# Kernel tuning notes

Hardware: AMD Instinct MI355X
Metric: run time of the kernel (lower is better)

The kernel has to match this reference:

```python
import jax, jax.numpy as jnp
import numpy as np

N_NODES = 50000
N_EDGES = 640000
D = 128
N_RELS = 16
N_NTYPES = 8


def setup_inputs() -> dict:
    key = jax.random.key(0)
    ks = jax.random.split(key, 9)
    return {
        "feats": jax.random.normal(ks[0], (N_NODES, D), dtype=jnp.float32),
        "W_edge": jax.random.normal(ks[1], (N_RELS, D, D), dtype=jnp.float32) / np.sqrt(D),
        "b_edge": jax.random.normal(ks[2], (N_RELS, D), dtype=jnp.float32) * 0.02,
        "W_node": jax.random.normal(ks[3], (N_NTYPES, D, D), dtype=jnp.float32) / np.sqrt(D),
        "b_node": jax.random.normal(ks[4], (N_NTYPES, D), dtype=jnp.float32) * 0.02,
        "src": jax.random.randint(ks[5], (N_EDGES,), 0, N_NODES, dtype=jnp.int32),
        "dst": jax.random.randint(ks[6], (N_EDGES,), 0, N_NODES, dtype=jnp.int32),
        "ntypes": jax.random.randint(ks[7], (N_NODES,), 0, N_NTYPES, dtype=jnp.int32),
        "etypes": jax.random.randint(ks[8], (N_EDGES,), 0, N_RELS, dtype=jnp.int32),
    }


def reference(feats, W_edge, b_edge, W_node, b_node, src, dst, ntypes, etypes):
    N, d = feats.shape
    T = W_edge.shape[0]
    # Per-relation linear applied to all nodes once: [T, N, out]; then gather per edge.
    hW = jnp.einsum('nd,tdf->tnf', feats, W_edge) + b_edge[:, None, :]
    msg = hW[etypes, src]  # [E, out]
    # Per-(dst-node, edge-type) in-degree counts (one_hot count normalization).
    seg = dst * T + etypes  # [E]
    counts = jax.ops.segment_sum(jnp.ones(msg.shape[0], dtype=msg.dtype), seg,
                                 num_segments=N * T)  # [N*T]
    msg = msg / counts[seg][:, None]
    # Scatter-sum messages into destination nodes (zero for isolated nodes).
    agg = jax.ops.segment_sum(msg, dst, num_segments=N)  # [N, out]
    # Type-conditional node transform + residual message + activation.
    hN = jnp.einsum('nd,tdf->tnf', feats, W_node) + b_node[:, None, :]  # [Tn, N, out]
    out = hN[ntypes, jnp.arange(N)] + agg
    return jax.nn.relu(out)
```

## Files before the change

kernel.cpp:

```cpp
#include <hip/hip_runtime.h>
#include <hip/hip_bf16.h>
#include <stdint.h>


#define D 128
#define TRELS 16
#define NTYPES 8

typedef __bf16 bf16x8 __attribute__((ext_vector_type(8)));
typedef float f32x4 __attribute__((ext_vector_type(4)));

__device__ __forceinline__ unsigned short f2bf(float f) {
  union { float f; unsigned u; } v; v.f = f;
  unsigned u = v.u;
  return (unsigned short)((u + 0x7FFFu + ((u >> 16) & 1u)) >> 16);
}
__device__ __forceinline__ float bf2f(unsigned short h) {
  union { unsigned u; float f; } v; v.u = ((unsigned)h) << 16;
  return v.f;
}

__global__ void prep_k(const float* __restrict__ feats,
                       const float* __restrict__ We,
                       const float* __restrict__ Wn,
                       unsigned short* __restrict__ featsbf,
                       unsigned short* __restrict__ WeT,
                       unsigned short* __restrict__ WnT,
                       int nfeat) {
  int idx = blockIdx.x * 256 + threadIdx.x;
  if (idx < nfeat) { featsbf[idx] = f2bf(feats[idx]); return; }
  idx -= nfeat;
  if (idx < TRELS * D * D) {
    int t = idx >> 14, rem = idx & 16383;
    int n = rem >> 7, k = rem & 127;
    WeT[idx] = f2bf(We[t * 16384 + k * 128 + n]);
    return;
  }
  idx -= TRELS * D * D;
  if (idx < NTYPES * D * D) {
    int t = idx >> 14, rem = idx & 16383;
    int n = rem >> 7, k = rem & 127;
    WnT[idx] = f2bf(Wn[t * 16384 + k * 128 + n]);
  }
}

__global__ void hist_k(const int* __restrict__ dst, const int* __restrict__ etypes,
                       const int* __restrict__ ntypes, int E, int N,
                       int* __restrict__ cnt, int* __restrict__ nhist) {
  __shared__ int sh_n[NTYPES];
  int tid = threadIdx.x;
  if (tid < NTYPES) sh_n[tid] = 0;
  __syncthreads();
  int g = blockIdx.x * 256 + tid;
  if (g < E) atomicAdd(&cnt[dst[g] * TRELS + etypes[g]], 1);
  if (g < N) atomicAdd(&sh_n[ntypes[g]], 1);
  __syncthreads();
  if (tid < NTYPES && sh_n[tid]) atomicAdd(&nhist[tid], sh_n[tid]);
}

__global__ void scan1_k(const int* __restrict__ cnt, int* __restrict__ doff,
                        int* __restrict__ bsum, int N) {
  __shared__ int sd[256];
  int b = blockIdx.x, tid = threadIdx.x;
  int base = b * 1024 + tid * 4;
  int v[4]; int tot = 0;
  for (int j = 0; j < 4; ++j) {
    int i = base + j;
    int dg = 0;
    if (i < N) {
      const int* row = cnt + i * TRELS;
#pragma unroll
      for (int et = 0; et < TRELS; ++et) dg += row[et];
    }
    v[j] = tot; tot += dg;
  }
  sd[tid] = tot;
  __syncthreads();
  for (int off = 1; off < 256; off <<= 1) {
    int t = (tid >= off) ? sd[tid - off] : 0;
    __syncthreads();
    sd[tid] += t;
    __syncthreads();
  }
  int excl = sd[tid] - tot;
  for (int j = 0; j < 4; ++j) {
    int i = base + j;
    if (i < N) doff[i] = excl + v[j];
  }
  if (tid == 255) bsum[b] = sd[255];
}

__global__ void scan2_k(int* __restrict__ misc, int* __restrict__ bsum, int nb) {
  if (threadIdx.x != 0) return;
  int run = 0;
  for (int b = 0; b < nb; ++b) { int t = bsum[b]; bsum[b] = run; run += t; }
  int* noff = misc; int* ntb = misc + 9; int* ncur = misc + 18; int* nhist = misc + 26;
  int s = 0, ts = 0;
  for (int t = 0; t < NTYPES; ++t) {
    noff[t] = s; ncur[t] = s; ntb[t] = ts;
    s += nhist[t]; ts += (nhist[t] + 127) >> 7;
  }
  noff[NTYPES] = s; ntb[NTYPES] = ts;
}

__global__ void scan3_k(int* __restrict__ doff, int* __restrict__ dcur,
                        const int* __restrict__ bsum, int N, int E) {
  int b = blockIdx.x, tid = threadIdx.x;
  int add = bsum[b];
  int base = b * 1024 + tid * 4;
  for (int j = 0; j < 4; ++j) {
    int i = base + j;
    if (i < N) { int o = doff[i] + add; doff[i] = o; dcur[i] = o; }
  }
  if (b == 0 && tid == 0) doff[N] = E;
}

__global__ void scatter_k(const int* __restrict__ src, const int* __restrict__ dst,
                          const int* __restrict__ etypes, const int* __restrict__ ntypes,
                          int E, int N, int* __restrict__ misc,
                          int* __restrict__ dcur,
                          int* __restrict__ edst, int* __restrict__ nsorted) {
  __shared__ int lc_n[NTYPES], lb_n[NTYPES];
  int tid = threadIdx.x;
  if (tid < NTYPES) lc_n[tid] = 0;
  __syncthreads();
  int g = blockIdx.x * 256 + tid;
  if (g < E) {
    int d = dst[g];
    int pos = atomicAdd(&dcur[d], 1);
    edst[pos] = src[g] * TRELS + etypes[g];
  }
  int tn = -1, idn = 0;
  if (g < N) { tn = ntypes[g]; idn = atomicAdd(&lc_n[tn], 1); }
  __syncthreads();
  if (tid < NTYPES && lc_n[tid]) lb_n[tid] = atomicAdd(&misc[18 + tid], lc_n[tid]);
  __syncthreads();
  if (g < N) nsorted[lb_n[tn] + idn] = g;
}

__global__ __launch_bounds__(256) void hw_gemm_k(
    const unsigned short* __restrict__ featsbf,
    const unsigned short* __restrict__ WeT,
    unsigned short* __restrict__ hW, int N) {
  __shared__ unsigned char Asm[128 * 264];
  int tid = threadIdx.x;
  int et = blockIdx.y;
  int tile = blockIdx.x;

  int lane = tid & 63, w = tid >> 6;
  int m = lane & 15, q = lane >> 4;
  int rw = (w & 1) * 64, cw = (w >> 1) * 64;

  const unsigned short* WB = WeT + et * (D * D);
  bf16x8 bfr[4][4];
#pragma unroll
  for (int ks = 0; ks < 4; ++ks)
#pragma unroll
    for (int j = 0; j < 4; ++j)
      bfr[ks][j] = *reinterpret_cast<const bf16x8*>(WB + (cw + j * 16 + m) * D + ks * 32 + q * 8);

  int r = tid >> 1, h = tid & 1;
  int row = tile * 128 + r;
  if (row < N) {
    const uint4* gp = reinterpret_cast<const uint4*>(featsbf + (size_t)row * D);
#pragma unroll
    for (int cc = 0; cc < 8; ++cc) {
      int c = h * 8 + cc;
      *reinterpret_cast<uint4*>(&Asm[r * 256 + ((c ^ (r & 7)) << 4)]) = gp[c];
    }
  }
  __syncthreads();

  f32x4 acc[4][4];
#pragma unroll
  for (int i = 0; i < 4; ++i)
#pragma unroll
    for (int j = 0; j < 4; ++j) acc[i][j] = (f32x4){0.f, 0.f, 0.f, 0.f};

#pragma unroll
  for (int ks = 0; ks < 4; ++ks) {
    bf16x8 a[4];
#pragma unroll
    for (int i = 0; i < 4; ++i) {
      int rr = rw + i * 16 + m;
      int c = ks * 4 + q;
      a[i] = *reinterpret_cast<const bf16x8*>(&Asm[rr * 256 + ((c ^ (rr & 7)) << 4)]);
    }
#pragma unroll
    for (int i = 0; i < 4; ++i)
#pragma unroll
      for (int j = 0; j < 4; ++j)
        acc[i][j] = __builtin_amdgcn_mfma_f32_16x16x32_bf16(a[i], bfr[ks][j], acc[i][j], 0, 0, 0);
  }

  __syncthreads();
  unsigned short* Cs = reinterpret_cast<unsigned short*>(Asm);
#pragma unroll
  for (int i = 0; i < 4; ++i)
#pragma unroll
    for (int j = 0; j < 4; ++j)
#pragma unroll
      for (int reg = 0; reg < 4; ++reg) {
        int rr = rw + i * 16 + q * 4 + reg;
        Cs[rr * 132 + cw + j * 16 + m] = f2bf(acc[i][j][reg]);
      }
  __syncthreads();
  char* gout = (char*)(hW + ((size_t)et * N + (size_t)tile * 128) * D);
#pragma unroll
  for (int cp = 0; cp < 8; ++cp) {
    int o = cp * 4096 + tid * 16;
    int rloc = o >> 8;
    if (tile * 128 + rloc < N) {
      uint4 v = *reinterpret_cast<const uint4*>(&Asm[rloc * 264 + (o & 255)]);
      *reinterpret_cast<uint4*>(gout + o) = v;
    }
  }
}

__global__ __launch_bounds__(256) void agg_k(
    const unsigned short* __restrict__ hW,
    const float* __restrict__ b_edge,
    const int* __restrict__ cnt,
    const int* __restrict__ doff, const int* __restrict__ edst,
    float* __restrict__ agg, int N) {
  int tid = threadIdx.x;
  int lane = tid & 63, w = tid >> 6;
  int d = blockIdx.x * 4 + w;
  if (d >= N) return;

  int cv = 0;
  if (lane < TRELS) cv = cnt[d * TRELS + lane];
  float invl = (cv > 0) ? 1.0f / (float)cv : 0.0f;

  int start = doff[d], end = doff[d + 1];
  float ax = 0.f, ay = 0.f;
  for (int base = start; base < end; base += 64) {
    int key = 0;
    if (base + lane < end) key = edst[base + lane];
    int nchunk = end - base; if (nchunk > 64) nchunk = 64;
    int j = 0;
    for (; j + 4 <= nchunk; j += 4) {
      int k0 = __shfl(key, j, 64), k1 = __shfl(key, j + 1, 64);
      int k2 = __shfl(key, j + 2, 64), k3 = __shfl(key, j + 3, 64);
      float i0 = __shfl(invl, k0 & 15, 64), i1 = __shfl(invl, k1 & 15, 64);
      float i2 = __shfl(invl, k2 & 15, 64), i3 = __shfl(invl, k3 & 15, 64);
      ushort2 h0 = *reinterpret_cast<const ushort2*>(hW + ((size_t)(k0 & 15) * N + (k0 >> 4)) * D + lane * 2);
      ushort2 h1 = *reinterpret_cast<const ushort2*>(hW + ((size_t)(k1 & 15) * N + (k1 >> 4)) * D + lane * 2);
      ushort2 h2 = *reinterpret_cast<const ushort2*>(hW + ((size_t)(k2 & 15) * N + (k2 >> 4)) * D + lane * 2);
      ushort2 h3 = *reinterpret_cast<const ushort2*>(hW + ((size_t)(k3 & 15) * N + (k3 >> 4)) * D + lane * 2);
      ax += i0 * bf2f(h0.x); ay += i0 * bf2f(h0.y);
      ax += i1 * bf2f(h1.x); ay += i1 * bf2f(h1.y);
      ax += i2 * bf2f(h2.x); ay += i2 * bf2f(h2.y);
      ax += i3 * bf2f(h3.x); ay += i3 * bf2f(h3.y);
    }
    for (; j < nchunk; ++j) {
      int k = __shfl(key, j, 64);
      float inv = __shfl(invl, k & 15, 64);
      ushort2 hv = *reinterpret_cast<const ushort2*>(hW + ((size_t)(k & 15) * N + (k >> 4)) * D + lane * 2);
      ax += inv * bf2f(hv.x); ay += inv * bf2f(hv.y);
    }
  }
#pragma unroll
  for (int et = 0; et < TRELS; ++et) {
    int c = __shfl(cv, et, 64);
    if (c > 0) {
      const float* bp = b_edge + et * D + lane * 2;
      ax += bp[0]; ay += bp[1];
    }
  }
  float2* op = reinterpret_cast<float2*>(agg + (size_t)d * D + lane * 2);
  *op = make_float2(ax, ay);
}

__global__ __launch_bounds__(256) void node_gemm_k(
    const unsigned short* __restrict__ featsbf,
    const unsigned short* __restrict__ WnT,
    const float* __restrict__ b_node,
    const int* __restrict__ nsorted, const int* __restrict__ misc,
    const float* __restrict__ agg,
    float* __restrict__ out) {
  __shared__ unsigned char Asm[128 * 264];
  __shared__ int sm_node[128];
  __shared__ int s_ntb[9];
  int tid = threadIdx.x;
  if (tid < 9) s_ntb[tid] = misc[9 + tid];
  __syncthreads();
  int bid = blockIdx.x;
  if (bid >= s_ntb[8]) return;
  int t = 0;
  while (bid >= s_ntb[t + 1]) ++t;
  int tile = bid - s_ntb[t];
  int noff_t = misc[t];
  int cntT = misc[t + 1] - noff_t;

  int lane = tid & 63, w = tid >> 6;
  int m = lane & 15, q = lane >> 4;
  int rw = (w & 1) * 64, cw = (w >> 1) * 64;

  const unsigned short* WB = WnT + t * (D * D);
  bf16x8 bfr[4][4];
#pragma unroll
  for (int ks = 0; ks < 4; ++ks)
#pragma unroll
    for (int j = 0; j < 4; ++j)
      bfr[ks][j] = *reinterpret_cast<const bf16x8*>(WB + (cw + j * 16 + m) * D + ks * 32 + q * 8);

  int r = tid >> 1, h = tid & 1;
  int gidx = tile * 128 + r;
  bool rv = gidx < cntT;
  int node = 0;
  if (rv) node = nsorted[noff_t + gidx];
  if (h == 0) sm_node[r] = rv ? node : -1;
  if (rv) {
    const uint4* gp = reinterpret_cast<const uint4*>(featsbf + (size_t)node * D);
#pragma unroll
    for (int cc = 0; cc < 8; ++cc) {
      int c = h * 8 + cc;
      *reinterpret_cast<uint4*>(&Asm[r * 256 + ((c ^ (r & 7)) << 4)]) = gp[c];
    }
  }
  __syncthreads();

  f32x4 acc[4][4];
#pragma unroll
  for (int i = 0; i < 4; ++i)
#pragma unroll
    for (int j = 0; j < 4; ++j) acc[i][j] = (f32x4){0.f, 0.f, 0.f, 0.f};

#pragma unroll
  for (int ks = 0; ks < 4; ++ks) {
    bf16x8 a[4];
#pragma unroll
    for (int i = 0; i < 4; ++i) {
      int rr = rw + i * 16 + m;
      int c = ks * 4 + q;
      a[i] = *reinterpret_cast<const bf16x8*>(&Asm[rr * 256 + ((c ^ (rr & 7)) << 4)]);
    }
#pragma unroll
    for (int i = 0; i < 4; ++i)
#pragma unroll
      for (int j = 0; j < 4; ++j)
        acc[i][j] = __builtin_amdgcn_mfma_f32_16x16x32_bf16(a[i], bfr[ks][j], acc[i][j], 0, 0, 0);
  }

  const float* bnp = b_node + t * D;
  float* Cf = reinterpret_cast<float*>(Asm);
  __syncthreads();
#pragma unroll
  for (int half = 0; half < 2; ++half) {
    if ((w & 1) == half) {
#pragma unroll
      for (int i = 0; i < 4; ++i)
#pragma unroll
        for (int j = 0; j < 4; ++j)
#pragma unroll
          for (int reg = 0; reg < 4; ++reg) {
            int rl = i * 16 + q * 4 + reg;
            Cf[rl * 132 + cw + j * 16 + m] = acc[i][j][reg];
          }
    }
    __syncthreads();
#pragma unroll
    for (int cp = 0; cp < 8; ++cp) {
      int o = cp * 4096 + tid * 16;
      int rl = o >> 9;
      int nd = sm_node[half * 64 + rl];
      if (nd >= 0) {
        int col = (o & 511) >> 2;
        f32x4 c = *reinterpret_cast<const f32x4*>((char*)Cf + rl * 528 + (o & 511));
        f32x4 a = *reinterpret_cast<const f32x4*>(agg + (size_t)nd * D + col);
        f32x4 b4 = *reinterpret_cast<const f32x4*>(bnp + col);
        f32x4 res;
#pragma unroll
        for (int z = 0; z < 4; ++z) res[z] = fmaxf(c[z] + a[z] + b4[z], 0.f);
        *reinterpret_cast<f32x4*>(out + (size_t)nd * D + col) = res;
      }
    }
    __syncthreads();
  }
}

static inline size_t align256(size_t x) { return (x + 255) & ~(size_t)255; }

extern "C" void kernel_launch(void* const* d_in, const int* in_sizes, int n_in,
                              void* d_out, int out_size, void* d_ws, size_t ws_size,
                              hipStream_t stream) {
  const float* feats  = (const float*)d_in[0];
  const float* W_edge = (const float*)d_in[1];
  const float* b_edge = (const float*)d_in[2];
  const float* W_node = (const float*)d_in[3];
  const float* b_node = (const float*)d_in[4];
  const int* src    = (const int*)d_in[5];
  const int* dst    = (const int*)d_in[6];
  const int* ntypes = (const int*)d_in[7];
  const int* etypes = (const int*)d_in[8];
  int N = in_sizes[0] / D;
  int E = in_sizes[5];

  char* ws = (char*)d_ws;
  size_t o_cnt  = 0;
  size_t o_misc = align256(o_cnt + (size_t)N * TRELS * 4);
  size_t zend   = align256(o_misc + 512);
  size_t o_doff = zend;
  size_t o_dcur = align256(o_doff + (size_t)(N + 1) * 4);
  size_t o_edst = align256(o_dcur + (size_t)N * 4);
  size_t o_ns   = align256(o_edst + (size_t)E * 4);
  size_t o_fb   = align256(o_ns + (size_t)N * 4);
  size_t o_we   = align256(o_fb + (size_t)N * D * 2);
  size_t o_wn   = align256(o_we + (size_t)TRELS * D * D * 2);
  size_t o_agg  = align256(o_wn + (size_t)NTYPES * D * D * 2);
  size_t o_hw   = align256(o_agg + (size_t)N * D * 4);

  int* cnt = (int*)(ws + o_cnt);
  int* misc = (int*)(ws + o_misc);
  int* doff = (int*)(ws + o_doff);
  int* dcur = (int*)(ws + o_dcur);
  int* edst = (int*)(ws + o_edst);
  int* nsorted = (int*)(ws + o_ns);
  unsigned short* featsbf = (unsigned short*)(ws + o_fb);
  unsigned short* WeT = (unsigned short*)(ws + o_we);
  unsigned short* WnT = (unsigned short*)(ws + o_wn);
  float* agg = (float*)(ws + o_agg);
  unsigned short* hW = (unsigned short*)(ws + o_hw);
  int* bsum = misc + 64;

  hipMemsetAsync(ws, 0, zend, stream);

  int nfeat = N * D;
  int ptot = nfeat + TRELS * D * D + NTYPES * D * D;
  prep_k<<<(ptot + 255) / 256, 256, 0, stream>>>(feats, W_edge, W_node, featsbf, WeT, WnT, nfeat);

  int hgrid = ((E > N ? E : N) + 255) / 256;
  hist_k<<<hgrid, 256, 0, stream>>>(dst, etypes, ntypes, E, N, cnt, misc + 26);

  int nb = (N + 1023) / 1024;
  scan1_k<<<nb, 256, 0, stream>>>(cnt, doff, bsum, N);
  scan2_k<<<1, 64, 0, stream>>>(misc, bsum, nb);
  scan3_k<<<nb, 256, 0, stream>>>(doff, dcur, bsum, N, E);

  scatter_k<<<hgrid, 256, 0, stream>>>(src, dst, etypes, ntypes, E, N, misc, dcur, edst, nsorted);

  int mtiles = (N + 127) / 128;
  dim3 ggrid(mtiles, TRELS);
  hw_gemm_k<<<ggrid, 256, 0, stream>>>(featsbf, WeT, hW, N);

  agg_k<<<(N + 3) / 4, 256, 0, stream>>>(hW, b_edge, cnt, doff, edst, agg, N);

  int ngrid = mtiles + NTYPES;
  node_gemm_k<<<ngrid, 256, 0, stream>>>(featsbf, WnT, b_node, nsorted, misc, agg, (float*)d_out);
}
```

Baseline: 344.5 us.

## Remap hw_gemm blocks per XCD, use nontemporal stores, widen agg gathers

Measured after the change: 347.4 us. Within noise of the previous version (+0.8%).

```diff
diff --git a/kernel.cpp b/kernel.cpp
--- a/kernel.cpp
+++ b/kernel.cpp
@@ -9,6 +9,7 @@
 
 typedef __bf16 bf16x8 __attribute__((ext_vector_type(8)));
 typedef float f32x4 __attribute__((ext_vector_type(4)));
+typedef unsigned int u32x4 __attribute__((ext_vector_type(4)));
 
 __device__ __forceinline__ unsigned short f2bf(float f) {
   union { float f; unsigned u; } v; v.f = f;
@@ -18,6 +19,11 @@
 __device__ __forceinline__ float bf2f(unsigned short h) {
   union { unsigned u; float f; } v; v.u = ((unsigned)h) << 16;
   return v.f;
+}
+__device__ __forceinline__ void bfpair(unsigned u, float& lo, float& hi) {
+  union { unsigned u; float f; } a, b;
+  a.u = u << 16; b.u = u & 0xffff0000u;
+  lo = a.f; hi = b.f;
 }
 
 __global__ void prep_k(const float* __restrict__ feats,
@@ -141,14 +147,20 @@
 __global__ __launch_bounds__(256) void hw_gemm_k(
     const unsigned short* __restrict__ featsbf,
     const unsigned short* __restrict__ WeT,
-    unsigned short* __restrict__ hW, int N) {
+    unsigned short* __restrict__ hW, int N, int mtiles) {
   __shared__ unsigned char Asm[128 * 264];
   int tid = threadIdx.x;
-  int et = blockIdx.y;
-  int tile = blockIdx.x;
+
+  int G = mtiles * 16;
+  int q = G >> 3, rmod = G & 7;
+  int xcd = blockIdx.x & 7, bidx = blockIdx.x >> 3;
+  int wrk = (xcd < rmod) ? (xcd * (q + 1) + bidx)
+                         : (rmod * (q + 1) + (xcd - rmod) * q + bidx);
+  int tile = wrk >> 4;
+  int et = wrk & 15;
 
   int lane = tid & 63, w = tid >> 6;
-  int m = lane & 15, q = lane >> 4;
+  int m = lane & 15, qd = lane >> 4;
   int rw = (w & 1) * 64, cw = (w >> 1) * 64;
 
   const unsigned short* WB = WeT + et * (D * D);
@@ -157,16 +169,16 @@
   for (int ks = 0; ks < 4; ++ks)
 #pragma unroll
     for (int j = 0; j < 4; ++j)
-      bfr[ks][j] = *reinterpret_cast<const bf16x8*>(WB + (cw + j * 16 + m) * D + ks * 32 + q * 8);
+      bfr[ks][j] = *reinterpret_cast<const bf16x8*>(WB + (cw + j * 16 + m) * D + ks * 32 + qd * 8);
 
   int r = tid >> 1, h = tid & 1;
   int row = tile * 128 + r;
   if (row < N) {
-    const uint4* gp = reinterpret_cast<const uint4*>(featsbf + (size_t)row * D);
+    const u32x4* gp = reinterpret_cast<const u32x4*>(featsbf + (size_t)row * D);
 #pragma unroll
     for (int cc = 0; cc < 8; ++cc) {
       int c = h * 8 + cc;
-      *reinterpret_cast<uint4*>(&Asm[r * 256 + ((c ^ (r & 7)) << 4)]) = gp[c];
+      *reinterpret_cast<u32x4*>(&Asm[r * 256 + ((c ^ (r & 7)) << 4)]) = gp[c];
     }
   }
   __syncthreads();
@@ -183,7 +195,7 @@
 #pragma unroll
     for (int i = 0; i < 4; ++i) {
       int rr = rw + i * 16 + m;
-      int c = ks * 4 + q;
+      int c = ks * 4 + qd;
       a[i] = *reinterpret_cast<const bf16x8*>(&Asm[rr * 256 + ((c ^ (rr & 7)) << 4)]);
     }
 #pragma unroll
@@ -201,7 +213,7 @@
     for (int j = 0; j < 4; ++j)
 #pragma unroll
       for (int reg = 0; reg < 4; ++reg) {
-        int rr = rw + i * 16 + q * 4 + reg;
+        int rr = rw + i * 16 + qd * 4 + reg;
         Cs[rr * 132 + cw + j * 16 + m] = f2bf(acc[i][j][reg]);
       }
   __syncthreads();
@@ -211,8 +223,8 @@
     int o = cp * 4096 + tid * 16;
     int rloc = o >> 8;
     if (tile * 128 + rloc < N) {
-      uint4 v = *reinterpret_cast<const uint4*>(&Asm[rloc * 264 + (o & 255)]);
-      *reinterpret_cast<uint4*>(gout + o) = v;
+      u32x4 v = *reinterpret_cast<const u32x4*>(&Asm[rloc * 264 + (o & 255)]);
+      __builtin_nontemporal_store(v, reinterpret_cast<u32x4*>(gout + o));
     }
   }
 }
@@ -232,44 +244,56 @@
   if (lane < TRELS) cv = cnt[d * TRELS + lane];
   float invl = (cv > 0) ? 1.0f / (float)cv : 0.0f;
 
+  int g = lane >> 4;
+  int sub = lane & 15;
+
   int start = doff[d], end = doff[d + 1];
-  float ax = 0.f, ay = 0.f;
+  float acc[8];
+#pragma unroll
+  for (int z = 0; z < 8; ++z) acc[z] = 0.f;
+
   for (int base = start; base < end; base += 64) {
     int key = 0;
     if (base + lane < end) key = edst[base + lane];
     int nchunk = end - base; if (nchunk > 64) nchunk = 64;
-    int j = 0;
-    for (; j + 4 <= nchunk; j += 4) {
-      int k0 = __shfl(key, j, 64), k1 = __shfl(key, j + 1, 64);
-      int k2 = __shfl(key, j + 2, 64), k3 = __shfl(key, j + 3, 64);
-      float i0 = __shfl(invl, k0 & 15, 64), i1 = __shfl(invl, k1 & 15, 64);
-      float i2 = __shfl(invl, k2 & 15, 64), i3 = __shfl(invl, k3 & 15, 64);
-      ushort2 h0 = *reinterpret_cast<const ushort2*>(hW + ((size_t)(k0 & 15) * N + (k0 >> 4)) * D + lane * 2);
-      ushort2 h1 = *reinterpret_cast<const ushort2*>(hW + ((size_t)(k1 & 15) * N + (k1 >> 4)) * D + lane * 2);
-      ushort2 h2 = *reinterpret_cast<const ushort2*>(hW + ((size_t)(k2 & 15) * N + (k2 >> 4)) * D + lane * 2);
-      ushort2 h3 = *reinterpret_cast<const ushort2*>(hW + ((size_t)(k3 & 15) * N + (k3 >> 4)) * D + lane * 2);
-      ax += i0 * bf2f(h0.x); ay += i0 * bf2f(h0.y);
-      ax += i1 * bf2f(h1.x); ay += i1 * bf2f(h1.y);
-      ax += i2 * bf2f(h2.x); ay += i2 * bf2f(h2.y);
-      ax += i3 * bf2f(h3.x); ay += i3 * bf2f(h3.y);
-    }
-    for (; j < nchunk; ++j) {
-      int k = __shfl(key, j, 64);
+#pragma unroll 2
+    for (int j = 0; j < nchunk; j += 4) {
+      int rr = j + g;
+      int k = __shfl(key, rr, 64);
       float inv = __shfl(invl, k & 15, 64);
-      ushort2 hv = *reinterpret_cast<const ushort2*>(hW + ((size_t)(k & 15) * N + (k >> 4)) * D + lane * 2);
-      ax += inv * bf2f(hv.x); ay += inv * bf2f(hv.y);
-    }
-  }
+      if (rr < nchunk) {
+        const unsigned short* hp =
+            hW + ((size_t)(k & 15) * N + (size_t)(k >> 4)) * D + sub * 8;
+        u32x4 hv = *reinterpret_cast<const u32x4*>(hp);
+        float lo, hi;
+        bfpair(hv.x, lo, hi); acc[0] += inv * lo; acc[1] += inv * hi;
+        bfpair(hv.y, lo, hi); acc[2] += inv * lo; acc[3] += inv * hi;
+        bfpair(hv.z, lo, hi); acc[4] += inv * lo; acc[5] += inv * hi;
+        bfpair(hv.w, lo, hi); acc[6] += inv * lo; acc[7] += inv * hi;
+      }
+    }
+  }
+
+#pragma unroll
+  for (int z = 0; z < 8; ++z) {
+    acc[z] += __shfl_xor(acc[z], 16, 64);
+    acc[z] += __shfl_xor(acc[z], 32, 64);
+  }
+
+  int cb = sub * 8 + (g & 1) * 4;
+  f32x4 res = { acc[(g & 1) * 4 + 0], acc[(g & 1) * 4 + 1],
+                acc[(g & 1) * 4 + 2], acc[(g & 1) * 4 + 3] };
 #pragma unroll
   for (int et = 0; et < TRELS; ++et) {
     int c = __shfl(cv, et, 64);
     if (c > 0) {
-      const float* bp = b_edge + et * D + lane * 2;
-      ax += bp[0]; ay += bp[1];
-    }
-  }
-  float2* op = reinterpret_cast<float2*>(agg + (size_t)d * D + lane * 2);
-  *op = make_float2(ax, ay);
+      f32x4 b4 = *reinterpret_cast<const f32x4*>(b_edge + et * D + cb);
+#pragma unroll
+      for (int z = 0; z < 4; ++z) res[z] += b4[z];
+    }
+  }
+  if (g < 2)
+    *reinterpret_cast<f32x4*>(agg + (size_t)d * D + cb) = res;
 }
 
 __global__ __launch_bounds__(256) void node_gemm_k(
@@ -312,11 +336,11 @@
   if (rv) node = nsorted[noff_t + gidx];
   if (h == 0) sm_node[r] = rv ? node : -1;
   if (rv) {
-    const uint4* gp = reinterpret_cast<const uint4*>(featsbf + (size_t)node * D);
+    const u32x4* gp = reinterpret_cast<const u32x4*>(featsbf + (size_t)node * D);
 #pragma unroll
     for (int cc = 0; cc < 8; ++cc) {
       int c = h * 8 + cc;
-      *reinterpret_cast<uint4*>(&Asm[r * 256 + ((c ^ (r & 7)) << 4)]) = gp[c];
+      *reinterpret_cast<u32x4*>(&Asm[r * 256 + ((c ^ (r & 7)) << 4)]) = gp[c];
     }
   }
   __syncthreads();
@@ -424,7 +448,7 @@
   unsigned short* hW = (unsigned short*)(ws + o_hw);
   int* bsum = misc + 64;
 
-  hipMemsetAsync(ws, 0, zend, stream);
+  (void)hipMemsetAsync(ws, 0, zend, stream);
 
   int nfeat = N * D;
   int ptot = nfeat + TRELS * D * D + NTYPES * D * D;
@@ -441,8 +465,7 @@
   scatter_k<<<hgrid, 256, 0, stream>>>(src, dst, etypes, ntypes, E, N, misc, dcur, edst, nsorted);
 
   int mtiles = (N + 127) / 128;
-  dim3 ggrid(mtiles, TRELS);
-  hw_gemm_k<<<ggrid, 256, 0, stream>>>(featsbf, WeT, hW, N);
+  hw_gemm_k<<<mtiles * 16, 256, 0, stream>>>(featsbf, WeT, hW, N, mtiles);
 
   agg_k<<<(N + 3) / 4, 256, 0, stream>>>(hW, b_edge, cnt, doff, edst, agg, N);
 
```

## Skip storing unused per-relation hW rows and remap GEMM blocks per XCD

Applied to the files above, without the earlier changes.

Result: no change. 349.5 us (+1.4%).

```diff
diff --git a/kernel.cpp b/kernel.cpp
--- a/kernel.cpp
+++ b/kernel.cpp
@@ -9,6 +9,7 @@
 
 typedef __bf16 bf16x8 __attribute__((ext_vector_type(8)));
 typedef float f32x4 __attribute__((ext_vector_type(4)));
+typedef unsigned int u32x4 __attribute__((ext_vector_type(4)));
 
 __device__ __forceinline__ unsigned short f2bf(float f) {
   union { float f; unsigned u; } v; v.f = f;
@@ -44,15 +45,21 @@
   }
 }
 
-__global__ void hist_k(const int* __restrict__ dst, const int* __restrict__ etypes,
+__global__ void hist_k(const int* __restrict__ src, const int* __restrict__ dst,
+                       const int* __restrict__ etypes,
                        const int* __restrict__ ntypes, int E, int N,
-                       int* __restrict__ cnt, int* __restrict__ nhist) {
+                       int* __restrict__ cnt, int* __restrict__ nhist,
+                       int* __restrict__ srcuse) {
   __shared__ int sh_n[NTYPES];
   int tid = threadIdx.x;
   if (tid < NTYPES) sh_n[tid] = 0;
   __syncthreads();
   int g = blockIdx.x * 256 + tid;
-  if (g < E) atomicAdd(&cnt[dst[g] * TRELS + etypes[g]], 1);
+  if (g < E) {
+    int et = etypes[g];
+    atomicAdd(&cnt[dst[g] * TRELS + et], 1);
+    atomicOr(&srcuse[src[g]], 1 << et);
+  }
   if (g < N) atomicAdd(&sh_n[ntypes[g]], 1);
   __syncthreads();
   if (tid < NTYPES && sh_n[tid]) atomicAdd(&nhist[tid], sh_n[tid]);
@@ -141,32 +148,45 @@
 __global__ __launch_bounds__(256) void hw_gemm_k(
     const unsigned short* __restrict__ featsbf,
     const unsigned short* __restrict__ WeT,
-    unsigned short* __restrict__ hW, int N) {
+    const int* __restrict__ srcuse,
+    unsigned short* __restrict__ hW, int N, int mtiles) {
   __shared__ unsigned char Asm[128 * 264];
+  __shared__ unsigned char sm_use[128];
   int tid = threadIdx.x;
-  int et = blockIdx.y;
-  int tile = blockIdx.x;
+
+  int G = mtiles * 16;
+  int q = G >> 3, rmod = G & 7;
+  int xcd = blockIdx.x & 7, bidx = blockIdx.x >> 3;
+  int wrk = (xcd < rmod) ? (xcd * (q + 1) + bidx)
+                         : (rmod * (q + 1) + (xcd - rmod) * q + bidx);
+  int tile = wrk >> 4;
+  int et = wrk & 15;
 
   int lane = tid & 63, w = tid >> 6;
-  int m = lane & 15, q = lane >> 4;
+  int m = lane & 15, qd = lane >> 4;
   int rw = (w & 1) * 64, cw = (w >> 1) * 64;
 
-  const unsigned short* WB = WeT + et * (D * D);
+  const unsigned short* WB = WeT + (size_t)et * (D * D);
   bf16x8 bfr[4][4];
 #pragma unroll
   for (int ks = 0; ks < 4; ++ks)
 #pragma unroll
     for (int j = 0; j < 4; ++j)
-      bfr[ks][j] = *reinterpret_cast<const bf16x8*>(WB + (cw + j * 16 + m) * D + ks * 32 + q * 8);
+      bfr[ks][j] = *reinterpret_cast<const bf16x8*>(WB + (cw + j * 16 + m) * D + ks * 32 + qd * 8);
+
+  if (tid < 128) {
+    int rowu = tile * 128 + tid;
+    sm_use[tid] = (rowu < N) ? (unsigned char)((srcuse[rowu] >> et) & 1) : 0;
+  }
 
   int r = tid >> 1, h = tid & 1;
   int row = tile * 128 + r;
   if (row < N) {
-    const uint4* gp = reinterpret_cast<const uint4*>(featsbf + (size_t)row * D);
+    const u32x4* gp = reinterpret_cast<const u32x4*>(featsbf + (size_t)row * D);
 #pragma unroll
     for (int cc = 0; cc < 8; ++cc) {
       int c = h * 8 + cc;
-      *reinterpret_cast<uint4*>(&Asm[r * 256 + ((c ^ (r & 7)) << 4)]) = gp[c];
+      *reinterpret_cast<u32x4*>(&Asm[r * 256 + ((c ^ (r & 7)) << 4)]) = gp[c];
     }
   }
   __syncthreads();
@@ -183,7 +203,7 @@
 #pragma unroll
     for (int i = 0; i < 4; ++i) {
       int rr = rw + i * 16 + m;
-      int c = ks * 4 + q;
+      int c = ks * 4 + qd;
       a[i] = *reinterpret_cast<const bf16x8*>(&Asm[rr * 256 + ((c ^ (rr & 7)) << 4)]);
     }
 #pragma unroll
@@ -201,7 +221,7 @@
     for (int j = 0; j < 4; ++j)
 #pragma unroll
       for (int reg = 0; reg < 4; ++reg) {
-        int rr = rw + i * 16 + q * 4 + reg;
+        int rr = rw + i * 16 + qd * 4 + reg;
         Cs[rr * 132 + cw + j * 16 + m] = f2bf(acc[i][j][reg]);
       }
   __syncthreads();
@@ -210,9 +230,9 @@
   for (int cp = 0; cp < 8; ++cp) {
     int o = cp * 4096 + tid * 16;
     int rloc = o >> 8;
-    if (tile * 128 + rloc < N) {
-      uint4 v = *reinterpret_cast<const uint4*>(&Asm[rloc * 264 + (o & 255)]);
-      *reinterpret_cast<uint4*>(gout + o) = v;
+    if (tile * 128 + rloc < N && sm_use[rloc]) {
+      u32x4 v = *reinterpret_cast<const u32x4*>(&Asm[rloc * 264 + (o & 255)]);
+      *reinterpret_cast<u32x4*>(gout + o) = v;
     }
   }
 }
@@ -312,11 +332,11 @@
   if (rv) node = nsorted[noff_t + gidx];
   if (h == 0) sm_node[r] = rv ? node : -1;
   if (rv) {
-    const uint4* gp = reinterpret_cast<const uint4*>(featsbf + (size_t)node * D);
+    const u32x4* gp = reinterpret_cast<const u32x4*>(featsbf + (size_t)node * D);
 #pragma unroll
     for (int cc = 0; cc < 8; ++cc) {
       int c = h * 8 + cc;
-      *reinterpret_cast<uint4*>(&Asm[r * 256 + ((c ^ (r & 7)) << 4)]) = gp[c];
+      *reinterpret_cast<u32x4*>(&Asm[r * 256 + ((c ^ (r & 7)) << 4)]) = gp[c];
     }
   }
   __syncthreads();
@@ -400,7 +420,8 @@
   char* ws = (char*)d_ws;
   size_t o_cnt  = 0;
   size_t o_misc = align256(o_cnt + (size_t)N * TRELS * 4);
-  size_t zend   = align256(o_misc + 512);
+  size_t o_su   = align256(o_misc + 512);
+  size_t zend   = align256(o_su + (size_t)N * 4);
   size_t o_doff = zend;
   size_t o_dcur = align256(o_doff + (size_t)(N + 1) * 4);
   size_t o_edst = align256(o_dcur + (size_t)N * 4);
@@ -413,6 +434,7 @@
 
   int* cnt = (int*)(ws + o_cnt);
   int* misc = (int*)(ws + o_misc);
+  int* srcuse = (int*)(ws + o_su);
   int* doff = (int*)(ws + o_doff);
   int* dcur = (int*)(ws + o_dcur);
   int* edst = (int*)(ws + o_edst);
@@ -424,14 +446,14 @@
   unsigned short* hW = (unsigned short*)(ws + o_hw);
   int* bsum = misc + 64;
 
-  hipMemsetAsync(ws, 0, zend, stream);
+  (void)hipMemsetAsync(ws, 0, zend, stream);
 
   int nfeat = N * D;
   int ptot = nfeat + TRELS * D * D + NTYPES * D * D;
   prep_k<<<(ptot + 255) / 256, 256, 0, stream>>>(feats, W_edge, W_node, featsbf, WeT, WnT, nfeat);
 
   int hgrid = ((E > N ? E : N) + 255) / 256;
-  hist_k<<<hgrid, 256, 0, stream>>>(dst, etypes, ntypes, E, N, cnt, misc + 26);
+  hist_k<<<hgrid, 256, 0, stream>>>(src, dst, etypes, ntypes, E, N, cnt, misc + 26, srcuse);
 
   int nb = (N + 1023) / 1024;
   scan1_k<<<nb, 256, 0, stream>>>(cnt, doff, bsum, N);
@@ -441,8 +463,7 @@
   scatter_k<<<hgrid, 256, 0, stream>>>(src, dst, etypes, ntypes, E, N, misc, dcur, edst, nsorted);
 
   int mtiles = (N + 127) / 128;
-  dim3 ggrid(mtiles, TRELS);
-  hw_gemm_k<<<ggrid, 256, 0, stream>>>(featsbf, WeT, hW, N);
+  hw_gemm_k<<<mtiles * 16, 256, 0, stream>>>(featsbf, WeT, srcuse, hW, N, mtiles);
 
   agg_k<<<(N + 3) / 4, 256, 0, stream>>>(hW, b_edge, cnt, doff, edst, agg, N);
 
```
